# Performance work log

Measured on AMD Instinct MI355X. Metric: run time of the kernel, lower is better.

Reference implementation:

```python
import jax, jax.numpy as jnp
import numpy as np
from jax import lax

B, L, D, H = 2, 4096, 1024, 16
K = 4            # short conv kernel size
HD = D // H      # head dim = 64
EPS = 1e-5


def causal_dw_conv(x, w):
    # depthwise causal conv: x [B,L,D], w [D,K]
    xp = jnp.pad(x, ((0, 0), (K - 1, 0), (0, 0)))
    out = xp[:, 0:L, :] * w[:, 0]
    for j in range(1, K):
        out = out + xp[:, j:j + L, :] * w[:, j]
    return out


def setup_inputs() -> dict:
    key = jax.random.key(0)
    ks = jax.random.split(key, 10)
    s = 0.02
    return {
        "hidden_states": jax.random.normal(ks[0], (B, L, D), jnp.float32),
        "Wq": jax.random.normal(ks[1], (D, D), jnp.float32) * s,
        "Wk": jax.random.normal(ks[2], (D, D), jnp.float32) * s,
        "Wv": jax.random.normal(ks[3], (D, D), jnp.float32) * s,
        "Wb": jax.random.normal(ks[4], (D, H), jnp.float32) * s,
        "conv_q": jax.random.normal(ks[5], (D, K), jnp.float32) * s,
        "conv_k": jax.random.normal(ks[6], (D, K), jnp.float32) * s,
        "conv_v": jax.random.normal(ks[7], (D, K), jnp.float32) * s,
        "o_norm_w": jnp.ones((HD,), jnp.float32),
        "Wo": jax.random.normal(ks[8], (D, D), jnp.float32) * s,
    }


def reference(hidden_states, Wq, Wk, Wv, Wb, conv_q, conv_k, conv_v, o_norm_w, Wo):
    x = hidden_states
    # projections + short causal conv with SiLU (qk_activation == 'silu')
    q = jax.nn.silu(causal_dw_conv(x @ Wq, conv_q))
    k = jax.nn.silu(causal_dw_conv(x @ Wk, conv_k))
    v = jax.nn.silu(causal_dw_conv(x @ Wv, conv_v))

    # [B,L,D] -> [L,B,H,hd] for the time scan
    def to_heads(t):
        return t.reshape(B, L, H, HD).transpose(1, 0, 2, 3)

    q, k, v = to_heads(q), to_heads(k), to_heads(v)

    # l2 qk-norm
    q = q / jnp.linalg.norm(q, axis=-1, keepdims=True)
    k = k / jnp.linalg.norm(k, axis=-1, keepdims=True)

    # beta gate [L,B,H]
    beta = jax.nn.sigmoid(x @ Wb).transpose(1, 0, 2)

    def step(S, inp):
        qt, kt, vt, bt = inp  # [B,H,hd] x3, [B,H]
        v_old = jnp.einsum('bhk,bhkv->bhv', kt, S)
        delta = (vt - v_old) * bt[..., None]
        S = S + jnp.einsum('bhk,bhv->bhkv', kt, delta)
        ot = jnp.einsum('bhk,bhkv->bhv', qt, S)
        return S, ot

    S0 = jnp.zeros((B, H, HD, HD), x.dtype)
    _, o = lax.scan(step, S0, (q, k, v, beta))  # o: [L,B,H,hd]
    o = o.transpose(1, 0, 2, 3)  # [B,L,H,hd]

    # per-head RMSNorm
    rms = jax.lax.rsqrt(jnp.mean(o * o, axis=-1, keepdims=True) + EPS)
    o = o * rms * o_norm_w

    return o.reshape(B, L, D) @ Wo
```

## Files before the change

### kernel.cpp

```cpp
#include <hip/hip_runtime.h>
#include <hip/hip_bf16.h>
#include <math.h>

#define BB 2
#define LL 4096
#define DD 1024
#define HH 16
#define HDIM 64
#define CC 64
#define NC 64
#define BH 32
#define GG 8
#define GS 8

typedef __attribute__((ext_vector_type(8))) short short8;
typedef __attribute__((ext_vector_type(4))) float f32x4;
typedef unsigned short u16;

__device__ __forceinline__ u16 f2bf(float f) {
    unsigned int u = __float_as_uint(f);
    unsigned int r = (u + 0x7fffu + ((u >> 16) & 1u)) >> 16;
    return (u16)r;
}
__device__ __forceinline__ float bf2f(u16 h) {
    return __uint_as_float((unsigned)h << 16);
}
__device__ __forceinline__ void split2(float x, u16& h, u16& l) {
    h = f2bf(x);
    l = f2bf(x - bf2f(h));
}

__device__ __forceinline__ void gld_lds16(const void* g, void* l) {
    __builtin_amdgcn_global_load_lds(
        (const __attribute__((address_space(1))) void*)g,
        (__attribute__((address_space(3))) void*)l, 16, 0, 0);
}

__device__ __forceinline__ int swz(int r, int c) {
    return (r << 6) + ((((c >> 2) ^ (r >> 2)) & 15) << 2) + (c & 3);
}
__device__ __forceinline__ int swze(int r, int c) {
    return (r << 6) + (c ^ (((r ^ (r >> 3)) & 7) << 3));
}

__device__ __forceinline__ void mm64(const u16* __restrict__ Ah, const u16* __restrict__ Al,
                                     const u16* __restrict__ Bh, const u16* __restrict__ Bl,
                                     f32x4* acc, int w, int lane) {
    const int ln = lane & 15, kg = (lane >> 4) * 8;
#pragma unroll
    for (int kb = 0; kb < 2; ++kb) {
        const int k0 = kb * 32 + kg;
        short8 ah = *(const short8*)&Ah[swze(w * 16 + ln, k0)];
        short8 al = *(const short8*)&Al[swze(w * 16 + ln, k0)];
#pragma unroll
        for (int j = 0; j < 4; ++j) {
            short8 bh = *(const short8*)&Bh[swze(j * 16 + ln, k0)];
            short8 bl = *(const short8*)&Bl[swze(j * 16 + ln, k0)];
            acc[j] = __builtin_amdgcn_mfma_f32_16x16x32_bf16(ah, bh, acc[j], 0, 0, 0);
            acc[j] = __builtin_amdgcn_mfma_f32_16x16x32_bf16(ah, bl, acc[j], 0, 0, 0);
            acc[j] = __builtin_amdgcn_mfma_f32_16x16x32_bf16(al, bh, acc[j], 0, 0, 0);
        }
    }
}

__device__ __forceinline__ void g_to_ls(const float* __restrict__ G, u16* Ah, u16* Al, int tid) {
#pragma unroll
    for (int p = 0; p < 4; ++p) {
        int flat = p * 1024 + tid * 4;
        int r = flat >> 6, c = flat & 63;
        float4 v = *(const float4*)&G[flat];
        u16 h0, l0, h1, l1, h2, l2, h3, l3;
        split2(v.x, h0, l0); split2(v.y, h1, l1);
        split2(v.z, h2, l2); split2(v.w, h3, l3);
        int idx = swze(r, c);
        uint2 hv, lv;
        hv.x = (unsigned)h0 | ((unsigned)h1 << 16); hv.y = (unsigned)h2 | ((unsigned)h3 << 16);
        lv.x = (unsigned)l0 | ((unsigned)l1 << 16); lv.y = (unsigned)l2 | ((unsigned)l3 << 16);
        *(uint2*)&Ah[idx] = hv;
        *(uint2*)&Al[idx] = lv;
    }
}

__device__ __forceinline__ void frag_to_ls(const f32x4* acc, u16* Ah, u16* Al, int w, int lane) {
    const int g = lane >> 4, ln = lane & 15;
#pragma unroll
    for (int j = 0; j < 4; ++j)
#pragma unroll
        for (int r = 0; r < 4; ++r) {
            int row = w * 16 + g * 4 + r, col = j * 16 + ln;
            u16 h, l; split2(acc[j][r], h, l);
            Ah[swze(row, col)] = h;
            Al[swze(row, col)] = l;
        }
}

__device__ __forceinline__ void g_to_frag(const float* __restrict__ G, f32x4* acc, int w, int lane) {
    const int g = lane >> 4, ln = lane & 15;
#pragma unroll
    for (int j = 0; j < 4; ++j)
#pragma unroll
        for (int r = 0; r < 4; ++r)
            acc[j][r] = G[(w * 16 + g * 4 + r) * 64 + j * 16 + ln];
}
__device__ __forceinline__ void g_add_frag(const float* __restrict__ G, f32x4* acc, int w, int lane) {
    const int g = lane >> 4, ln = lane & 15;
#pragma unroll
    for (int j = 0; j < 4; ++j)
#pragma unroll
        for (int r = 0; r < 4; ++r)
            acc[j][r] += G[(w * 16 + g * 4 + r) * 64 + j * 16 + ln];
}
__device__ __forceinline__ void frag_to_g(const f32x4* acc, float* __restrict__ G, int w, int lane) {
    const int g = lane >> 4, ln = lane & 15;
#pragma unroll
    for (int j = 0; j < 4; ++j)
#pragma unroll
        for (int r = 0; r < 4; ++r)
            G[(w * 16 + g * 4 + r) * 64 + j * 16 + ln] = acc[j][r];
}

__global__ __launch_bounds__(256) void cast_bf16_k(const float* __restrict__ in,
                                                   u16* __restrict__ out) {
    int i = (blockIdx.x * 256 + threadIdx.x) * 8;
    float4 a = *(const float4*)&in[i];
    float4 b = *(const float4*)&in[i + 4];
    uint4 o;
    o.x = (unsigned)f2bf(a.x) | ((unsigned)f2bf(a.y) << 16);
    o.y = (unsigned)f2bf(a.z) | ((unsigned)f2bf(a.w) << 16);
    o.z = (unsigned)f2bf(b.x) | ((unsigned)f2bf(b.y) << 16);
    o.w = (unsigned)f2bf(b.z) | ((unsigned)f2bf(b.w) << 16);
    *(uint4*)&out[i] = o;
}

__global__ __launch_bounds__(256) void transW4_k(const float* __restrict__ W0,
                                                 const float* __restrict__ W1,
                                                 const float* __restrict__ W2,
                                                 const float* __restrict__ W3,
                                                 u16* __restrict__ WT0) {
    __shared__ float t[32][33];
    const int which = blockIdx.z;
    const float* W = (which == 0) ? W0 : (which == 1) ? W1 : (which == 2) ? W2 : W3;
    u16* WT = WT0 + (size_t)which * 1048576;
    const int bx = blockIdx.x * 32, by = blockIdx.y * 32;
#pragma unroll
    for (int p = 0; p < 4; ++p) {
        int idx = p * 256 + threadIdx.x;
        int r = idx >> 5, cc = idx & 31;
        t[r][cc] = W[(size_t)(by + r) * 1024 + bx + cc];
    }
    __syncthreads();
#pragma unroll
    for (int p = 0; p < 4; ++p) {
        int idx = p * 256 + threadIdx.x;
        int r = idx >> 5, cc = idx & 31;
        WT[(size_t)(bx + r) * 1024 + by + cc] = f2bf(t[cc][r]);
    }
}

__device__ __forceinline__ void gemm_body(const u16* A, const u16* BT,
                                          float* C, int m0, int n0) {
    __shared__ __align__(16) short As[128 * 32];
    __shared__ __align__(16) short Bs[128 * 32];
    const int tid = threadIdx.x;
    const int lane = tid & 63, w = tid >> 6;
    const int wr = w >> 1, wc = w & 1;
    const int ln15 = lane & 15, kg8 = (lane >> 4) * 8;
    f32x4 acc[4][4] = {};
    const int erow = tid >> 2;
    const int ecol = (tid & 3) * 8;
    for (int k0 = 0; k0 < 1024; k0 += 32) {
#pragma unroll
        for (int r = 0; r < 2; ++r) {
            gld_lds16(A  + (size_t)(m0 + erow + r * 64) * 1024 + k0 + ecol,
                      (short*)As + r * 2048 + tid * 8);
            gld_lds16(BT + (size_t)(n0 + erow + r * 64) * 1024 + k0 + ecol,
                      (short*)Bs + r * 2048 + tid * 8);
        }
        __syncthreads();
        short8 af[4], bf[4];
#pragma unroll
        for (int i = 0; i < 4; ++i)
            af[i] = *(const short8*)&As[(wr * 64 + i * 16 + ln15) * 32 + kg8];
#pragma unroll
        for (int j = 0; j < 4; ++j)
            bf[j] = *(const short8*)&Bs[(wc * 64 + j * 16 + ln15) * 32 + kg8];
#pragma unroll
        for (int i = 0; i < 4; ++i)
#pragma unroll
            for (int j = 0; j < 4; ++j)
                acc[i][j] = __builtin_amdgcn_mfma_f32_16x16x32_bf16(af[i], bf[j], acc[i][j], 0, 0, 0);
        __syncthreads();
    }
    const int crow0 = m0 + wr * 64 + (lane >> 4) * 4;
    const int ccol0 = n0 + wc * 64 + ln15;
#pragma unroll
    for (int i = 0; i < 4; ++i)
#pragma unroll
        for (int j = 0; j < 4; ++j)
#pragma unroll
            for (int r = 0; r < 4; ++r)
                C[(size_t)(crow0 + i * 16 + r) * 1024 + ccol0 + j * 16] = acc[i][j][r];
}

__global__ __launch_bounds__(256) void gemm_bf16(const u16* __restrict__ A,
                                                 const u16* __restrict__ BT,
                                                 float* __restrict__ C) {
    gemm_body(A, BT, C, blockIdx.y * 128, blockIdx.x * 128);
}

__global__ __launch_bounds__(256) void gemm_qkv(const u16* __restrict__ A,
                                                const u16* __restrict__ WT0,
                                                float* __restrict__ C0) {
    const int which = blockIdx.x >> 3;
    const int n0 = (blockIdx.x & 7) * 128;
    const u16* BT = WT0 + (size_t)which * 1048576;
    float* C = C0 + (size_t)which * ((size_t)BB * LL * DD);
    gemm_body(A, BT, C, blockIdx.y * 128, n0);
}

__global__ __launch_bounds__(256) void beta_k(const float* __restrict__ X,
                                              const float* __restrict__ Wb,
                                              float* __restrict__ beta) {
    int idx = blockIdx.x * 256 + threadIdx.x;
    int row = idx >> 4, h = idx & 15;
    const float* xr = X + (size_t)row * DD;
    float s = 0.f;
    for (int k4 = 0; k4 < DD; k4 += 4) {
        float4 xv = *(const float4*)&xr[k4];
        s += xv.x * Wb[(k4 + 0) * HH + h];
        s += xv.y * Wb[(k4 + 1) * HH + h];
        s += xv.z * Wb[(k4 + 2) * HH + h];
        s += xv.w * Wb[(k4 + 3) * HH + h];
    }
    float bv = 1.f / (1.f + expf(-s));
    int b = row >> 12, l = row & (LL - 1);
    beta[((size_t)b * HH + h) * LL + l] = bv;
}

__global__ __launch_bounds__(256) void conv3_k(const float* __restrict__ Xq,
                                               const float* __restrict__ Xk,
                                               const float* __restrict__ Xv,
                                               const float* __restrict__ cwq,
                                               const float* __restrict__ cwk,
                                               const float* __restrict__ cwv,
                                               float* __restrict__ oq,
                                               float* __restrict__ ok,
                                               float* __restrict__ ov) {
    const int which = blockIdx.z;
    const float* X  = (which == 0) ? Xq  : (which == 1) ? Xk  : Xv;
    const float* cw = (which == 0) ? cwq : (which == 1) ? cwk : cwv;
    float* out      = (which == 0) ? oq  : (which == 1) ? ok  : ov;
    const bool NORM = (which < 2);
    const int l0 = blockIdx.x * 16, b = blockIdx.y;
    const int tid = threadIdx.x;
    const int d0 = tid * 4;
    const float4 w0 = *(const float4*)&cw[(d0 + 0) * 4];
    const float4 w1 = *(const float4*)&cw[(d0 + 1) * 4];
    const float4 w2 = *(const float4*)&cw[(d0 + 2) * 4];
    const float4 w3 = *(const float4*)&cw[(d0 + 3) * 4];
    const float* Xb = X + (size_t)b * LL * DD;
    float4 xm3 = make_float4(0, 0, 0, 0), xm2 = xm3, xm1 = xm3;
    if (l0 > 0) {
        xm3 = *(const float4*)&Xb[(size_t)(l0 - 3) * DD + d0];
        xm2 = *(const float4*)&Xb[(size_t)(l0 - 2) * DD + d0];
        xm1 = *(const float4*)&Xb[(size_t)(l0 - 1) * DD + d0];
    }
    const int h = d0 >> 6, hd = d0 & 63;
#pragma unroll
    for (int t = 0; t < 16; ++t) {
        const int l = l0 + t;
        float4 xc = *(const float4*)&Xb[(size_t)l * DD + d0];
        float a0 = xm3.x * w0.x + xm2.x * w0.y + xm1.x * w0.z + xc.x * w0.w;
        float a1 = xm3.y * w1.x + xm2.y * w1.y + xm1.y * w1.z + xc.y * w1.w;
        float a2 = xm3.z * w2.x + xm2.z * w2.y + xm1.z * w2.z + xc.z * w2.w;
        float a3 = xm3.w * w3.x + xm2.w * w3.y + xm1.w * w3.z + xc.w * w3.w;
        a0 = a0 / (1.f + expf(-a0));
        a1 = a1 / (1.f + expf(-a1));
        a2 = a2 / (1.f + expf(-a2));
        a3 = a3 / (1.f + expf(-a3));
        if (NORM) {
            float s = a0 * a0 + a1 * a1 + a2 * a2 + a3 * a3;
            s += __shfl_xor(s, 1);
            s += __shfl_xor(s, 2);
            s += __shfl_xor(s, 4);
            s += __shfl_xor(s, 8);
            float sc = rsqrtf(s);
            a0 *= sc; a1 *= sc; a2 *= sc; a3 *= sc;
        }
        *(float4*)&out[(((size_t)b * HH + h) * LL + l) * 64 + hd] =
            make_float4(a0, a1, a2, a3);
        xm3 = xm2; xm2 = xm1; xm1 = xc;
    }
}

__global__ __launch_bounds__(256) void phaseA4(const float* __restrict__ kg,
                                               const float* __restrict__ vg,
                                               const float* __restrict__ betag,
                                               float* __restrict__ Wg,
                                               float* __restrict__ UgT,
                                               float* __restrict__ Pall,
                                               float* __restrict__ BallT) {
    __shared__ __align__(16) char pool[81920];
    u16* Kh  = (u16*)pool;
    u16* Kl  = (u16*)(pool + 8192);
    u16* KTh = (u16*)(pool + 16384);
    u16* KTl = (u16*)(pool + 24576);
    float* At = (float*)(pool + 32768);
    float* WU = (float*)(pool + 49152);
    u16* WTh = (u16*)pool;
    u16* WTl = (u16*)(pool + 8192);
    u16* UTh = (u16*)(pool + 32768);
    u16* UTl = (u16*)(pool + 40960);
    float* scr = (float*)(pool + 49152);

    const int c = blockIdx.x, bh = blockIdx.y;
    const int tid = threadIdx.x, lane = tid & 63, w = tid >> 6;
    const int g = lane >> 4, ln = lane & 15;
    const int t0 = (tid >> 4) * 4, d4 = (tid & 15) * 4;
    const size_t base = ((size_t)bh * LL + (size_t)c * 64) * 64;
    const size_t obase = ((size_t)bh * NC + c) * 4096;
    const float* bet = betag + (size_t)bh * LL + (size_t)c * 64;

    g_to_ls(&kg[base], Kh, Kl, tid);
    {
        u16 h4[4][4], l4[4][4];
#pragma unroll
        for (int i = 0; i < 4; ++i) {
            float4 v = *(const float4*)&kg[base + (size_t)(t0 + i) * 64 + d4];
            split2(v.x, h4[i][0], l4[i][0]); split2(v.y, h4[i][1], l4[i][1]);
            split2(v.z, h4[i][2], l4[i][2]); split2(v.w, h4[i][3], l4[i][3]);
        }
#pragma unroll
        for (int j = 0; j < 4; ++j) {
            uint2 hv, lv;
            hv.x = (unsigned)h4[0][j] | ((unsigned)h4[1][j] << 16);
            hv.y = (unsigned)h4[2][j] | ((unsigned)h4[3][j] << 16);
            lv.x = (unsigned)l4[0][j] | ((unsigned)l4[1][j] << 16);
            lv.y = (unsigned)l4[2][j] | ((unsigned)l4[3][j] << 16);
            *(uint2*)&KTh[swze(d4 + j, t0)] = hv;
            *(uint2*)&KTl[swze(d4 + j, t0)] = lv;
        }
    }
    __syncthreads();
    {
        f32x4 acc[4] = {};
        mm64(Kh, Kl, Kh, Kl, acc, w, lane);
#pragma unroll
        for (int r = 0; r < 4; ++r) {
            int t = w * 16 + g * 4 + r;
            float bt = bet[t];
#pragma unroll
            for (int j = 0; j < 4; ++j) {
                int s = j * 16 + ln;
                At[t * 64 + s] = (s < t) ? bt * acc[j][r] : 0.f;
            }
        }
    }
#pragma unroll
    for (int p = 0; p < 8; ++p) {
        int flat = p * 1024 + tid * 4;
        int t = flat >> 7, j = flat & 127;
        float bt = bet[t];
        float4 src;
        if (j < 64) {
            int idx = swze(t, j);
            uint2 hh = *(const uint2*)&Kh[idx];
            uint2 ll2 = *(const uint2*)&Kl[idx];
            src.x = bf2f((u16)hh.x) + bf2f((u16)ll2.x);
            src.y = bf2f((u16)(hh.x >> 16)) + bf2f((u16)(ll2.x >> 16));
            src.z = bf2f((u16)hh.y) + bf2f((u16)ll2.y);
            src.w = bf2f((u16)(hh.y >> 16)) + bf2f((u16)(ll2.y >> 16));
        } else {
            src = *(const float4*)&vg[base + (size_t)t * 64 + (j - 64)];
        }
        src.x *= bt; src.y *= bt; src.z *= bt; src.w *= bt;
        *(float4*)&WU[t * 128 + j] = src;
    }
    __syncthreads();
#pragma unroll
    for (int pb = 0; pb < 4; ++pb) {
        const int r0 = pb * 16;
        if (pb > 0) {
            const int col = tid & 127;
            const int rbase = r0 + (tid >> 7) * 8;
            float acc8[8] = {};
            for (int r = 0; r < r0; r += 4) {
                float u0 = WU[(r + 0) * 128 + col], u1 = WU[(r + 1) * 128 + col];
                float u2 = WU[(r + 2) * 128 + col], u3 = WU[(r + 3) * 128 + col];
#pragma unroll
                for (int i = 0; i < 8; ++i) {
                    float4 a4 = *(const float4*)&At[(rbase + i) * 64 + r];
                    acc8[i] += a4.x * u0 + a4.y * u1 + a4.z * u2 + a4.w * u3;
                }
            }
#pragma unroll
            for (int i = 0; i < 8; ++i) WU[(rbase + i) * 128 + col] -= acc8[i];
            __syncthreads();
        }
        if (tid < 128) {
            const int col = tid;
            float wv[16];
            wv[0] = WU[r0 * 128 + col];
#pragma unroll
            for (int t = 1; t < 16; ++t) {
                float a = WU[(r0 + t) * 128 + col];
#pragma unroll
                for (int r = 0; r < t; ++r) a -= At[(r0 + t) * 64 + r0 + r] * wv[r];
                wv[t] = a;
            }
#pragma unroll
            for (int t = 1; t < 16; ++t) WU[(r0 + t) * 128 + col] = wv[t];
        }
        __syncthreads();
    }
#pragma unroll
    for (int p = 0; p < 4; ++p) {
        int flat = p * 1024 + tid * 4;
        int t = flat >> 6, j = flat & 63;
        *(float4*)&Wg[obase + flat] = *(const float4*)&WU[t * 128 + j];
    }
    {
        u16 h4[4][4], l4[4][4];
#pragma unroll
        for (int i = 0; i < 4; ++i) {
            float4 v = *(const float4*)&WU[(t0 + i) * 128 + d4];
            split2(v.x, h4[i][0], l4[i][0]); split2(v.y, h4[i][1], l4[i][1]);
            split2(v.z, h4[i][2], l4[i][2]); split2(v.w, h4[i][3], l4[i][3]);
        }
#pragma unroll
        for (int j = 0; j < 4; ++j) {
            uint2 hv, lv;
            hv.x = (unsigned)h4[0][j] | ((unsigned)h4[1][j] << 16);
            hv.y = (unsigned)h4[2][j] | ((unsigned)h4[3][j] << 16);
            lv.x = (unsigned)l4[0][j] | ((unsigned)l4[1][j] << 16);
            lv.y = (unsigned)l4[2][j] | ((unsigned)l4[3][j] << 16);
            *(uint2*)&WTh[swze(d4 + j, t0)] = hv;
            *(uint2*)&WTl[swze(d4 + j, t0)] = lv;
        }
#pragma unroll
        for (int i = 0; i < 4; ++i) {
            float4 v = *(const float4*)&WU[(t0 + i) * 128 + 64 + d4];
            split2(v.x, h4[i][0], l4[i][0]); split2(v.y, h4[i][1], l4[i][1]);
            split2(v.z, h4[i][2], l4[i][2]); split2(v.w, h4[i][3], l4[i][3]);
        }
#pragma unroll
        for (int j = 0; j < 4; ++j) {
            uint2 hv, lv;
            hv.x = (unsigned)h4[0][j] | ((unsigned)h4[1][j] << 16);
            hv.y = (unsigned)h4[2][j] | ((unsigned)h4[3][j] << 16);
            lv.x = (unsigned)l4[0][j] | ((unsigned)l4[1][j] << 16);
            lv.y = (unsigned)l4[2][j] | ((unsigned)l4[3][j] << 16);
            *(uint2*)&UTh[swze(d4 + j, t0)] = hv;
            *(uint2*)&UTl[swze(d4 + j, t0)] = lv;
        }
    }
    __syncthreads();
#pragma unroll
    for (int p = 0; p < 4; ++p) {
        int flat = p * 1024 + tid * 4;
        int n = flat >> 6, tt = flat & 63;
        int idx = swze(n, tt);
        uint2 hh = *(const uint2*)&UTh[idx];
        uint2 ll2 = *(const uint2*)&UTl[idx];
        float4 o;
        o.x = bf2f((u16)hh.x) + bf2f((u16)ll2.x);
        o.y = bf2f((u16)(hh.x >> 16)) + bf2f((u16)(ll2.x >> 16));
        o.z = bf2f((u16)hh.y) + bf2f((u16)ll2.y);
        o.w = bf2f((u16)(hh.y >> 16)) + bf2f((u16)(ll2.y >> 16));
        *(float4*)&UgT[obase + flat] = o;
    }
    f32x4 aP[4] = {}, aB[4] = {};
    mm64(KTh, KTl, WTh, WTl, aP, w, lane);
    mm64(KTh, KTl, UTh, UTl, aB, w, lane);
#pragma unroll
    for (int j = 0; j < 4; ++j)
#pragma unroll
        for (int r = 0; r < 4; ++r) {
            int row = w * 16 + g * 4 + r, col = j * 16 + ln;
            float pv = ((row == col) ? 1.f : 0.f) - aP[j][r];
            Pall[obase + (size_t)row * 64 + col] = pv;
            scr[swz(row, col)] = aB[j][r];
        }
    __syncthreads();
#pragma unroll
    for (int p = 0; p < 4; ++p) {
        int flat = p * 1024 + tid * 4;
        int n = flat >> 6, dd = flat & 63;
        float4 o;
        o.x = scr[swz(dd + 0, n)];
        o.y = scr[swz(dd + 1, n)];
        o.z = scr[swz(dd + 2, n)];
        o.w = scr[swz(dd + 3, n)];
        *(float4*)&BallT[obase + flat] = o;
    }
}

__global__ __launch_bounds__(256) void compose3(const float* __restrict__ Pall,
                                                const float* __restrict__ BallT,
                                                float* __restrict__ Pg,
                                                float* __restrict__ BgT) {
    __shared__ __align__(16) char pool[81920];
    u16* Ph = (u16*)pool;
    u16* Pl = (u16*)(pool + 8192);
    u16* Bh = (u16*)(pool + 16384);
    u16* Bl = (u16*)(pool + 24576);
    u16* nh = (u16*)(pool + 32768);
    u16* nl = (u16*)(pool + 40960);
    float* scr = (float*)(pool + 49152);
    const int g = blockIdx.x, bh = blockIdx.y;
    const int tid = threadIdx.x, lane = tid & 63, w = tid >> 6;
    const int gi = lane >> 4, ln = lane & 15;
    const size_t base0 = ((size_t)bh * NC + (size_t)g * GS) * 4096;
    f32x4 mP[4], mB[4];
#pragma unroll
    for (int p = 0; p < 4; ++p) {
        int flat = p * 1024 + tid * 4;
        int r = flat >> 6, c4 = flat & 63;
        *(float4*)&scr[swz(r, c4)] = *(const float4*)&Pall[base0 + flat];
    }
    g_to_frag(BallT + base0, mB, w, lane);
    __syncthreads();
#pragma unroll
    for (int j = 0; j < 4; ++j)
#pragma unroll
        for (int r = 0; r < 4; ++r) {
            int row = w * 16 + gi * 4 + r, col = j * 16 + ln;
            mP[j][r] = scr[swz(col, row)];
        }
    for (int s = 1; s < GS; ++s) {
        __syncthreads();
        frag_to_ls(mP, Ph, Pl, w, lane);
        frag_to_ls(mB, Bh, Bl, w, lane);
        g_to_ls(&Pall[base0 + (size_t)s * 4096], nh, nl, tid);
        __syncthreads();
        f32x4 aP[4] = {}, aB[4] = {};
        mm64(Ph, Pl, nh, nl, aP, w, lane);
        mm64(Bh, Bl, nh, nl, aB, w, lane);
        g_add_frag(&BallT[base0 + (size_t)s * 4096], aB, w, lane);
#pragma unroll
        for (int j = 0; j < 4; ++j) { mP[j] = aP[j]; mB[j] = aB[j]; }
    }
    const size_t gbase = ((size_t)bh * GG + g) * 4096;
    frag_to_g(mB, BgT + gbase, w, lane);
    __syncthreads();
#pragma unroll
    for (int j = 0; j < 4; ++j)
#pragma unroll
        for (int r = 0; r < 4; ++r) {
            int row = w * 16 + gi * 4 + r, col = j * 16 + ln;
            scr[swz(row, col)] = mP[j][r];
        }
    __syncthreads();
#pragma unroll
    for (int p = 0; p < 4; ++p) {
        int flat = p * 1024 + tid * 4;
        int a = flat >> 6, b0 = flat & 63;
        float4 o;
        o.x = scr[swz(b0 + 0, a)];
        o.y = scr[swz(b0 + 1, a)];
        o.z = scr[swz(b0 + 2, a)];
        o.w = scr[swz(b0 + 3, a)];
        *(float4*)&Pg[gbase + flat] = o;
    }
}

__global__ __launch_bounds__(256) void scanG3(const float* __restrict__ Pg,
                                              const float* __restrict__ BgT,
                                              float* __restrict__ SallT) {
    __shared__ __align__(16) char pool[32768];
    u16* Sh = (u16*)pool;
    u16* Sl = (u16*)(pool + 8192);
    u16* nh = (u16*)(pool + 16384);
    u16* nl = (u16*)(pool + 24576);
    const int bh = blockIdx.x;
    const int tid = threadIdx.x, lane = tid & 63, w = tid >> 6;
    f32x4 mS[4] = {};
    for (int g = 0; g < GG; ++g) {
        const size_t sbase = ((size_t)bh * NC + (size_t)g * GS) * 4096;
        frag_to_g(mS, SallT + sbase, w, lane);
        if (g == GG - 1) break;
        __syncthreads();
        frag_to_ls(mS, Sh, Sl, w, lane);
        g_to_ls(&Pg[((size_t)bh * GG + g) * 4096], nh, nl, tid);
        __syncthreads();
        f32x4 a[4] = {};
        mm64(Sh, Sl, nh, nl, a, w, lane);
        g_add_frag(&BgT[((size_t)bh * GG + g) * 4096], a, w, lane);
#pragma unroll
        for (int j = 0; j < 4; ++j) mS[j] = a[j];
    }
}

__global__ __launch_bounds__(256) void rollout3(const float* __restrict__ Pall,
                                                const float* __restrict__ BallT,
                                                float* __restrict__ SallT) {
    __shared__ __align__(16) char pool[32768];
    u16* Sh = (u16*)pool;
    u16* Sl = (u16*)(pool + 8192);
    u16* nh = (u16*)(pool + 16384);
    u16* nl = (u16*)(pool + 24576);
    const int g = blockIdx.x, bh = blockIdx.y;
    const int tid = threadIdx.x, lane = tid & 63, w = tid >> 6;
    const size_t base0 = ((size_t)bh * NC + (size_t)g * GS) * 4096;
    f32x4 mS[4];
    g_to_frag(SallT + base0, mS, w, lane);
    for (int j = 1; j < GS; ++j) {
        __syncthreads();
        frag_to_ls(mS, Sh, Sl, w, lane);
        g_to_ls(&Pall[base0 + (size_t)(j - 1) * 4096], nh, nl, tid);
        __syncthreads();
        f32x4 a[4] = {};
        mm64(Sh, Sl, nh, nl, a, w, lane);
        g_add_frag(&BallT[base0 + (size_t)(j - 1) * 4096], a, w, lane);
#pragma unroll
        for (int jj = 0; jj < 4; ++jj) mS[jj] = a[jj];
        frag_to_g(mS, SallT + base0 + (size_t)j * 4096, w, lane);
    }
}

__global__ __launch_bounds__(256) void phaseO3(const float* __restrict__ Wg,
                                               const float* __restrict__ UgT,
                                               const float* __restrict__ qg,
                                               const float* __restrict__ kg,
                                               const float* __restrict__ SallT,
                                               const float* __restrict__ nw,
                                               u16* __restrict__ ob) {
    __shared__ __align__(16) char pool[65536];
    u16* Qh = (u16*)pool;
    u16* Ql = (u16*)(pool + 8192);
    u16* Kh = (u16*)(pool + 16384);
    u16* Kl = (u16*)(pool + 24576);
    u16* Wh = (u16*)(pool + 32768);
    u16* Wl = (u16*)(pool + 40960);
    u16* Sh = (u16*)(pool + 49152);
    u16* Sl = (u16*)(pool + 57344);
    u16* Dh = Kh; u16* Dl = Kl;
    u16* Mh = Wh; u16* Ml = Wl;
    const int c = blockIdx.x, bh = blockIdx.y;
    const int b = bh >> 4, h = bh & 15;
    const int tid = threadIdx.x, lane = tid & 63, w = tid >> 6;
    const int gi = lane >> 4, ln = lane & 15;
    const size_t tbase = ((size_t)bh * NC + c) * 4096;
    const size_t qkbase = ((size_t)bh * LL + (size_t)c * 64) * 64;
    g_to_ls(&qg[qkbase], Qh, Ql, tid);
    g_to_ls(&kg[qkbase], Kh, Kl, tid);
    g_to_ls(&Wg[tbase], Wh, Wl, tid);
    g_to_ls(&SallT[tbase], Sh, Sl, tid);
    __syncthreads();
    f32x4 aM[4] = {}, aD[4] = {};
    mm64(Qh, Ql, Kh, Kl, aM, w, lane);
    mm64(Sh, Sl, Wh, Wl, aD, w, lane);
    __syncthreads();
#pragma unroll
    for (int j = 0; j < 4; ++j)
#pragma unroll
        for (int r = 0; r < 4; ++r) {
            int row = w * 16 + gi * 4 + r, col = j * 16 + ln;
            float mv = (col <= row) ? aM[j][r] : 0.f;
            u16 mh_, ml_; split2(mv, mh_, ml_);
            Mh[swze(row, col)] = mh_;
            Ml[swze(row, col)] = ml_;
            float dv = UgT[tbase + (size_t)row * 64 + col] - aD[j][r];
            u16 dh_, dl_; split2(dv, dh_, dl_);
            Dh[swze(row, col)] = dh_;
            Dl[swze(row, col)] = dl_;
        }
    __syncthreads();
    f32x4 aO[4] = {};
    mm64(Qh, Ql, Sh, Sl, aO, w, lane);
    mm64(Mh, Ml, Dh, Dl, aO, w, lane);
    float nwv[4];
#pragma unroll
    for (int j = 0; j < 4; ++j) nwv[j] = nw[j * 16 + ln];
#pragma unroll
    for (int r = 0; r < 4; ++r) {
        float ss = 0.f;
#pragma unroll
        for (int j = 0; j < 4; ++j) ss += aO[j][r] * aO[j][r];
        ss += __shfl_xor(ss, 1);
        ss += __shfl_xor(ss, 2);
        ss += __shfl_xor(ss, 4);
        ss += __shfl_xor(ss, 8);
        float rms = rsqrtf(ss * (1.f / 64.f) + 1e-5f);
        int row = w * 16 + gi * 4 + r;
        size_t orow = ((size_t)b * LL + (size_t)c * 64 + row) * DD + (size_t)h * 64;
#pragma unroll
        for (int j = 0; j < 4; ++j)
            ob[orow + j * 16 + ln] = f2bf(aO[j][r] * rms * nwv[j]);
    }
}

extern "C" void kernel_launch(void* const* d_in, const int* in_sizes, int n_in,
                              void* d_out, int out_size, void* d_ws, size_t ws_size,
                              hipStream_t stream) {
    const float* x  = (const float*)d_in[0];
    const float* Wq = (const float*)d_in[1];
    const float* Wk = (const float*)d_in[2];
    const float* Wv = (const float*)d_in[3];
    const float* Wb = (const float*)d_in[4];
    const float* cq = (const float*)d_in[5];
    const float* ck = (const float*)d_in[6];
    const float* cv = (const float*)d_in[7];
    const float* nw = (const float*)d_in[8];
    const float* Wo = (const float*)d_in[9];
    float* out = (float*)d_out;
    float* ws = (float*)d_ws;

    const size_t SZ = (size_t)BB * LL * DD;
    float* xq   = ws;
    float* xk   = ws + SZ;
    float* xv   = ws + 2 * SZ;
    float* q    = ws + 3 * SZ;
    float* k    = ws + 4 * SZ;
    float* v    = ws + 5 * SZ;
    float* beta = ws + 6 * SZ;
    u16* wqT = (u16*)(beta + (size_t)BH * LL);
    float* SallT = (float*)wqT + 2097152;
    float* PgB  = SallT + SZ;
    float* BgT  = PgB + 1048576;

    u16* xb = (u16*)q;
    u16* ob = (u16*)v;
    u16* woT = wqT + (size_t)3 * 1048576;
    float* Wg = xq;
    float* UgT = xk;
    float* Pall = xv;
    float* BallT = out;

    dim3 blk(256);

    cast_bf16_k<<<dim3(4096), blk, 0, stream>>>(x, xb);
    transW4_k<<<dim3(32, 32, 4), blk, 0, stream>>>(Wq, Wk, Wv, Wo, wqT);
    gemm_qkv<<<dim3(24, 64), blk, 0, stream>>>(xb, wqT, xq);
    beta_k<<<dim3(512), blk, 0, stream>>>(x, Wb, beta);
    conv3_k<<<dim3(LL / 16, BB, 3), blk, 0, stream>>>(xq, xk, xv, cq, ck, cv, q, k, v);
    phaseA4<<<dim3(NC, BH), blk, 0, stream>>>(k, v, beta, Wg, UgT, Pall, BallT);
    compose3<<<dim3(GG, BH), blk, 0, stream>>>(Pall, BallT, PgB, BgT);
    scanG3<<<dim3(BH), blk, 0, stream>>>(PgB, BgT, SallT);
    rollout3<<<dim3(GG, BH), blk, 0, stream>>>(Pall, BallT, SallT);
    phaseO3<<<dim3(NC, BH), blk, 0, stream>>>(Wg, UgT, q, k, SallT, nw, ob);
    gemm_bf16<<<dim3(8, 64), blk, 0, stream>>>(ob, woT, out);
}
```

Measured before the change: 387.0 us.

## Store q/k intermediates in bf16 and drop split-precision MFMA terms for them

The QKV GEMM now writes the q and k projections as bf16, the conv kernel reads bf16 and writes normalized q/k as bf16, and the chunk kernels load them directly without hi/lo splitting. Products involving only q/k use a single bf16 MFMA instead of three, and mixed products use two. This cuts memory traffic, LDS footprint and MFMA count in conv, phaseA and phaseO. The GEMM LDS tiles also gain an XOR swizzle to reduce bank conflicts. The cost is lower precision in q/k, which risks accuracy drift through the recurrent delta-rule state.

Result: faster. 363.1 us (-6.2%).

```diff
diff --git a/kernel.cpp b/kernel.cpp
--- a/kernel.cpp
+++ b/kernel.cpp
@@ -29,6 +29,11 @@
     h = f2bf(x);
     l = f2bf(x - bf2f(h));
 }
+__device__ __forceinline__ float4 ld_bf4(const u16* p) {
+    uint2 v = *(const uint2*)p;
+    return make_float4(bf2f((u16)v.x), bf2f((u16)(v.x >> 16)),
+                       bf2f((u16)v.y), bf2f((u16)(v.y >> 16)));
+}
 
 __device__ __forceinline__ void gld_lds16(const void* g, void* l) {
     __builtin_amdgcn_global_load_lds(
@@ -59,6 +64,38 @@
             acc[j] = __builtin_amdgcn_mfma_f32_16x16x32_bf16(ah, bh, acc[j], 0, 0, 0);
             acc[j] = __builtin_amdgcn_mfma_f32_16x16x32_bf16(ah, bl, acc[j], 0, 0, 0);
             acc[j] = __builtin_amdgcn_mfma_f32_16x16x32_bf16(al, bh, acc[j], 0, 0, 0);
+        }
+    }
+}
+__device__ __forceinline__ void mm64_bb(const u16* __restrict__ Ah,
+                                        const u16* __restrict__ Bh,
+                                        f32x4* acc, int w, int lane) {
+    const int ln = lane & 15, kg = (lane >> 4) * 8;
+#pragma unroll
+    for (int kb = 0; kb < 2; ++kb) {
+        const int k0 = kb * 32 + kg;
+        short8 ah = *(const short8*)&Ah[swze(w * 16 + ln, k0)];
+#pragma unroll
+        for (int j = 0; j < 4; ++j) {
+            short8 bh = *(const short8*)&Bh[swze(j * 16 + ln, k0)];
+            acc[j] = __builtin_amdgcn_mfma_f32_16x16x32_bf16(ah, bh, acc[j], 0, 0, 0);
+        }
+    }
+}
+__device__ __forceinline__ void mm64_ab(const u16* __restrict__ Ah,
+                                        const u16* __restrict__ Bh, const u16* __restrict__ Bl,
+                                        f32x4* acc, int w, int lane) {
+    const int ln = lane & 15, kg = (lane >> 4) * 8;
+#pragma unroll
+    for (int kb = 0; kb < 2; ++kb) {
+        const int k0 = kb * 32 + kg;
+        short8 ah = *(const short8*)&Ah[swze(w * 16 + ln, k0)];
+#pragma unroll
+        for (int j = 0; j < 4; ++j) {
+            short8 bh = *(const short8*)&Bh[swze(j * 16 + ln, k0)];
+            short8 bl = *(const short8*)&Bl[swze(j * 16 + ln, k0)];
+            acc[j] = __builtin_amdgcn_mfma_f32_16x16x32_bf16(ah, bh, acc[j], 0, 0, 0);
+            acc[j] = __builtin_amdgcn_mfma_f32_16x16x32_bf16(ah, bl, acc[j], 0, 0, 0);
         }
     }
 }
@@ -80,6 +117,14 @@
         *(uint2*)&Al[idx] = lv;
     }
 }
+__device__ __forceinline__ void g_to_ls_b(const u16* __restrict__ G16, u16* Ah, int tid) {
+#pragma unroll
+    for (int p = 0; p < 2; ++p) {
+        int flat = p * 2048 + tid * 8;
+        int r = flat >> 6, c = flat & 63;
+        *(short8*)&Ah[swze(r, c)] = *(const short8*)&G16[flat];
+    }
+}
 
 __device__ __forceinline__ void frag_to_ls(const f32x4* acc, u16* Ah, u16* Al, int w, int lane) {
     const int g = lane >> 4, ln = lane & 15;
@@ -157,17 +202,17 @@
     }
 }
 
-__device__ __forceinline__ void gemm_body(const u16* A, const u16* BT,
-                                          float* C, int m0, int n0) {
+__device__ __forceinline__ void gemm_core(const u16* A, const u16* BT,
+                                          int m0, int n0, f32x4 acc[4][4]) {
     __shared__ __align__(16) short As[128 * 32];
     __shared__ __align__(16) short Bs[128 * 32];
     const int tid = threadIdx.x;
     const int lane = tid & 63, w = tid >> 6;
     const int wr = w >> 1, wc = w & 1;
-    const int ln15 = lane & 15, kg8 = (lane >> 4) * 8;
-    f32x4 acc[4][4] = {};
+    const int ln15 = lane & 15;
     const int erow = tid >> 2;
-    const int ecol = (tid & 3) * 8;
+    const int ecol = (((tid & 3) ^ ((erow >> 1) & 3)) << 3);
+    const int kch = lane >> 4;
     for (int k0 = 0; k0 < 1024; k0 += 32) {
 #pragma unroll
         for (int r = 0; r < 2; ++r) {
@@ -179,11 +224,15 @@
         __syncthreads();
         short8 af[4], bf[4];
 #pragma unroll
-        for (int i = 0; i < 4; ++i)
-            af[i] = *(const short8*)&As[(wr * 64 + i * 16 + ln15) * 32 + kg8];
-#pragma unroll
-        for (int j = 0; j < 4; ++j)
-            bf[j] = *(const short8*)&Bs[(wc * 64 + j * 16 + ln15) * 32 + kg8];
+        for (int i = 0; i < 4; ++i) {
+            int row = wr * 64 + i * 16 + ln15;
+            af[i] = *(const short8*)&As[row * 32 + ((kch ^ ((row >> 1) & 3)) << 3)];
+        }
+#pragma unroll
+        for (int j = 0; j < 4; ++j) {
+            int row = wc * 64 + j * 16 + ln15;
+            bf[j] = *(const short8*)&Bs[row * 32 + ((kch ^ ((row >> 1) & 3)) << 3)];
+        }
 #pragma unroll
         for (int i = 0; i < 4; ++i)
 #pragma unroll
@@ -191,31 +240,58 @@
                 acc[i][j] = __builtin_amdgcn_mfma_f32_16x16x32_bf16(af[i], bf[j], acc[i][j], 0, 0, 0);
         __syncthreads();
     }
-    const int crow0 = m0 + wr * 64 + (lane >> 4) * 4;
-    const int ccol0 = n0 + wc * 64 + ln15;
-#pragma unroll
-    for (int i = 0; i < 4; ++i)
-#pragma unroll
-        for (int j = 0; j < 4; ++j)
-#pragma unroll
-            for (int r = 0; r < 4; ++r)
-                C[(size_t)(crow0 + i * 16 + r) * 1024 + ccol0 + j * 16] = acc[i][j][r];
 }
 
 __global__ __launch_bounds__(256) void gemm_bf16(const u16* __restrict__ A,
                                                  const u16* __restrict__ BT,
                                                  float* __restrict__ C) {
-    gemm_body(A, BT, C, blockIdx.y * 128, blockIdx.x * 128);
+    const int m0 = blockIdx.y * 128, n0 = blockIdx.x * 128;
+    f32x4 acc[4][4] = {};
+    gemm_core(A, BT, m0, n0, acc);
+    const int lane = threadIdx.x & 63, w = threadIdx.x >> 6;
+    const int crow0 = m0 + (w >> 1) * 64 + (lane >> 4) * 4;
+    const int ccol0 = n0 + (w & 1) * 64 + (lane & 15);
+#pragma unroll
+    for (int i = 0; i < 4; ++i)
+#pragma unroll
+        for (int j = 0; j < 4; ++j)
+#pragma unroll
+            for (int r = 0; r < 4; ++r)
+                C[(size_t)(crow0 + i * 16 + r) * 1024 + ccol0 + j * 16] = acc[i][j][r];
 }
 
 __global__ __launch_bounds__(256) void gemm_qkv(const u16* __restrict__ A,
                                                 const u16* __restrict__ WT0,
-                                                float* __restrict__ C0) {
+                                                u16* __restrict__ xq16,
+                                                u16* __restrict__ xk16,
+                                                float* __restrict__ xv) {
     const int which = blockIdx.x >> 3;
     const int n0 = (blockIdx.x & 7) * 128;
+    const int m0 = blockIdx.y * 128;
     const u16* BT = WT0 + (size_t)which * 1048576;
-    float* C = C0 + (size_t)which * ((size_t)BB * LL * DD);
-    gemm_body(A, BT, C, blockIdx.y * 128, n0);
+    f32x4 acc[4][4] = {};
+    gemm_core(A, BT, m0, n0, acc);
+    const int lane = threadIdx.x & 63, w = threadIdx.x >> 6;
+    const int crow0 = m0 + (w >> 1) * 64 + (lane >> 4) * 4;
+    const int ccol0 = n0 + (w & 1) * 64 + (lane & 15);
+    if (which == 2) {
+#pragma unroll
+        for (int i = 0; i < 4; ++i)
+#pragma unroll
+            for (int j = 0; j < 4; ++j)
+#pragma unroll
+                for (int r = 0; r < 4; ++r)
+                    xv[(size_t)(crow0 + i * 16 + r) * 1024 + ccol0 + j * 16] = acc[i][j][r];
+    } else {
+        u16* C16 = (which == 0) ? xq16 : xk16;
+#pragma unroll
+        for (int i = 0; i < 4; ++i)
+#pragma unroll
+            for (int j = 0; j < 4; ++j)
+#pragma unroll
+                for (int r = 0; r < 4; ++r)
+                    C16[(size_t)(crow0 + i * 16 + r) * 1024 + ccol0 + j * 16] = f2bf(acc[i][j][r]);
+    }
 }
 
 __global__ __launch_bounds__(256) void beta_k(const float* __restrict__ X,
@@ -237,20 +313,17 @@
     beta[((size_t)b * HH + h) * LL + l] = bv;
 }
 
-__global__ __launch_bounds__(256) void conv3_k(const float* __restrict__ Xq,
-                                               const float* __restrict__ Xk,
-                                               const float* __restrict__ Xv,
+__global__ __launch_bounds__(256) void conv3_k(const u16* __restrict__ xq16,
+                                               const u16* __restrict__ xk16,
+                                               const float* __restrict__ xv,
                                                const float* __restrict__ cwq,
                                                const float* __restrict__ cwk,
                                                const float* __restrict__ cwv,
-                                               float* __restrict__ oq,
-                                               float* __restrict__ ok,
-                                               float* __restrict__ ov) {
+                                               u16* __restrict__ q16,
+                                               u16* __restrict__ k16,
+                                               float* __restrict__ vout) {
     const int which = blockIdx.z;
-    const float* X  = (which == 0) ? Xq  : (which == 1) ? Xk  : Xv;
     const float* cw = (which == 0) ? cwq : (which == 1) ? cwk : cwv;
-    float* out      = (which == 0) ? oq  : (which == 1) ? ok  : ov;
-    const bool NORM = (which < 2);
     const int l0 = blockIdx.x * 16, b = blockIdx.y;
     const int tid = threadIdx.x;
     const int d0 = tid * 4;
@@ -258,27 +331,28 @@
     const float4 w1 = *(const float4*)&cw[(d0 + 1) * 4];
     const float4 w2 = *(const float4*)&cw[(d0 + 2) * 4];
     const float4 w3 = *(const float4*)&cw[(d0 + 3) * 4];
-    const float* Xb = X + (size_t)b * LL * DD;
-    float4 xm3 = make_float4(0, 0, 0, 0), xm2 = xm3, xm1 = xm3;
-    if (l0 > 0) {
-        xm3 = *(const float4*)&Xb[(size_t)(l0 - 3) * DD + d0];
-        xm2 = *(const float4*)&Xb[(size_t)(l0 - 2) * DD + d0];
-        xm1 = *(const float4*)&Xb[(size_t)(l0 - 1) * DD + d0];
-    }
     const int h = d0 >> 6, hd = d0 & 63;
-#pragma unroll
-    for (int t = 0; t < 16; ++t) {
-        const int l = l0 + t;
-        float4 xc = *(const float4*)&Xb[(size_t)l * DD + d0];
-        float a0 = xm3.x * w0.x + xm2.x * w0.y + xm1.x * w0.z + xc.x * w0.w;
-        float a1 = xm3.y * w1.x + xm2.y * w1.y + xm1.y * w1.z + xc.y * w1.w;
-        float a2 = xm3.z * w2.x + xm2.z * w2.y + xm1.z * w2.z + xc.z * w2.w;
-        float a3 = xm3.w * w3.x + xm2.w * w3.y + xm1.w * w3.z + xc.w * w3.w;
-        a0 = a0 / (1.f + expf(-a0));
-        a1 = a1 / (1.f + expf(-a1));
-        a2 = a2 / (1.f + expf(-a2));
-        a3 = a3 / (1.f + expf(-a3));
-        if (NORM) {
+    if (which < 2) {
+        const u16* Xb = ((which == 0) ? xq16 : xk16) + (size_t)b * LL * DD;
+        u16* O16 = (which == 0) ? q16 : k16;
+        float4 xm3 = make_float4(0, 0, 0, 0), xm2 = xm3, xm1 = xm3;
+        if (l0 > 0) {
+            xm3 = ld_bf4(&Xb[(size_t)(l0 - 3) * DD + d0]);
+            xm2 = ld_bf4(&Xb[(size_t)(l0 - 2) * DD + d0]);
+            xm1 = ld_bf4(&Xb[(size_t)(l0 - 1) * DD + d0]);
+        }
+#pragma unroll
+        for (int t = 0; t < 16; ++t) {
+            const int l = l0 + t;
+            float4 xc = ld_bf4(&Xb[(size_t)l * DD + d0]);
+            float a0 = xm3.x * w0.x + xm2.x * w0.y + xm1.x * w0.z + xc.x * w0.w;
+            float a1 = xm3.y * w1.x + xm2.y * w1.y + xm1.y * w1.z + xc.y * w1.w;
+            float a2 = xm3.z * w2.x + xm2.z * w2.y + xm1.z * w2.z + xc.z * w2.w;
+            float a3 = xm3.w * w3.x + xm2.w * w3.y + xm1.w * w3.z + xc.w * w3.w;
+            a0 = a0 / (1.f + expf(-a0));
+            a1 = a1 / (1.f + expf(-a1));
+            a2 = a2 / (1.f + expf(-a2));
+            a3 = a3 / (1.f + expf(-a3));
             float s = a0 * a0 + a1 * a1 + a2 * a2 + a3 * a3;
             s += __shfl_xor(s, 1);
             s += __shfl_xor(s, 2);
@@ -286,32 +360,56 @@
             s += __shfl_xor(s, 8);
             float sc = rsqrtf(s);
             a0 *= sc; a1 *= sc; a2 *= sc; a3 *= sc;
-        }
-        *(float4*)&out[(((size_t)b * HH + h) * LL + l) * 64 + hd] =
-            make_float4(a0, a1, a2, a3);
-        xm3 = xm2; xm2 = xm1; xm1 = xc;
-    }
-}
-
-__global__ __launch_bounds__(256) void phaseA4(const float* __restrict__ kg,
+            uint2 o;
+            o.x = (unsigned)f2bf(a0) | ((unsigned)f2bf(a1) << 16);
+            o.y = (unsigned)f2bf(a2) | ((unsigned)f2bf(a3) << 16);
+            *(uint2*)&O16[(((size_t)b * HH + h) * LL + l) * 64 + hd] = o;
+            xm3 = xm2; xm2 = xm1; xm1 = xc;
+        }
+    } else {
+        const float* Xb = xv + (size_t)b * LL * DD;
+        float4 xm3 = make_float4(0, 0, 0, 0), xm2 = xm3, xm1 = xm3;
+        if (l0 > 0) {
+            xm3 = *(const float4*)&Xb[(size_t)(l0 - 3) * DD + d0];
+            xm2 = *(const float4*)&Xb[(size_t)(l0 - 2) * DD + d0];
+            xm1 = *(const float4*)&Xb[(size_t)(l0 - 1) * DD + d0];
+        }
+#pragma unroll
+        for (int t = 0; t < 16; ++t) {
+            const int l = l0 + t;
+            float4 xc = *(const float4*)&Xb[(size_t)l * DD + d0];
+            float a0 = xm3.x * w0.x + xm2.x * w0.y + xm1.x * w0.z + xc.x * w0.w;
+            float a1 = xm3.y * w1.x + xm2.y * w1.y + xm1.y * w1.z + xc.y * w1.w;
+            float a2 = xm3.z * w2.x + xm2.z * w2.y + xm1.z * w2.z + xc.z * w2.w;
+            float a3 = xm3.w * w3.x + xm2.w * w3.y + xm1.w * w3.z + xc.w * w3.w;
+            a0 = a0 / (1.f + expf(-a0));
+            a1 = a1 / (1.f + expf(-a1));
+            a2 = a2 / (1.f + expf(-a2));
+            a3 = a3 / (1.f + expf(-a3));
+            *(float4*)&vout[(((size_t)b * HH + h) * LL + l) * 64 + hd] =
+                make_float4(a0, a1, a2, a3);
+            xm3 = xm2; xm2 = xm1; xm1 = xc;
+        }
+    }
+}
+
+__global__ __launch_bounds__(256) void phaseA5(const u16* __restrict__ kg16,
                                                const float* __restrict__ vg,
                                                const float* __restrict__ betag,
                                                float* __restrict__ Wg,
                                                float* __restrict__ UgT,
                                                float* __restrict__ Pall,
                                                float* __restrict__ BallT) {
-    __shared__ __align__(16) char pool[81920];
-    u16* Kh  = (u16*)pool;
-    u16* Kl  = (u16*)(pool + 8192);
-    u16* KTh = (u16*)(pool + 16384);
-    u16* KTl = (u16*)(pool + 24576);
-    float* At = (float*)(pool + 32768);
-    float* WU = (float*)(pool + 49152);
-    u16* WTh = (u16*)pool;
-    u16* WTl = (u16*)(pool + 8192);
-    u16* UTh = (u16*)(pool + 32768);
-    u16* UTl = (u16*)(pool + 40960);
-    float* scr = (float*)(pool + 49152);
+    __shared__ __align__(16) char pool[73728];
+    u16* Kh   = (u16*)pool;
+    u16* KTh  = (u16*)(pool + 8192);
+    float* At = (float*)(pool + 16384);
+    float* WU = (float*)(pool + 32768);
+    u16* WTh  = (u16*)pool;
+    u16* WTl  = (u16*)(pool + 16384);
+    u16* UTh  = (u16*)(pool + 24576);
+    u16* UTl  = (u16*)(pool + 65536);
+    float* scr = (float*)(pool + 32768);
 
     const int c = blockIdx.x, bh = blockIdx.y;
     const int tid = threadIdx.x, lane = tid & 63, w = tid >> 6;
@@ -321,30 +419,27 @@
     const size_t obase = ((size_t)bh * NC + c) * 4096;
     const float* bet = betag + (size_t)bh * LL + (size_t)c * 64;
 
-    g_to_ls(&kg[base], Kh, Kl, tid);
+    g_to_ls_b(kg16 + base, Kh, tid);
     {
-        u16 h4[4][4], l4[4][4];
+        u16 kv[4][4];
 #pragma unroll
         for (int i = 0; i < 4; ++i) {
-            float4 v = *(const float4*)&kg[base + (size_t)(t0 + i) * 64 + d4];
-            split2(v.x, h4[i][0], l4[i][0]); split2(v.y, h4[i][1], l4[i][1]);
-            split2(v.z, h4[i][2], l4[i][2]); split2(v.w, h4[i][3], l4[i][3]);
+            uint2 v = *(const uint2*)&kg16[base + (size_t)(t0 + i) * 64 + d4];
+            kv[i][0] = (u16)v.x; kv[i][1] = (u16)(v.x >> 16);
+            kv[i][2] = (u16)v.y; kv[i][3] = (u16)(v.y >> 16);
         }
 #pragma unroll
         for (int j = 0; j < 4; ++j) {
-            uint2 hv, lv;
-            hv.x = (unsigned)h4[0][j] | ((unsigned)h4[1][j] << 16);
-            hv.y = (unsigned)h4[2][j] | ((unsigned)h4[3][j] << 16);
-            lv.x = (unsigned)l4[0][j] | ((unsigned)l4[1][j] << 16);
-            lv.y = (unsigned)l4[2][j] | ((unsigned)l4[3][j] << 16);
+            uint2 hv;
+            hv.x = (unsigned)kv[0][j] | ((unsigned)kv[1][j] << 16);
+            hv.y = (unsigned)kv[2][j] | ((unsigned)kv[3][j] << 16);
             *(uint2*)&KTh[swze(d4 + j, t0)] = hv;
-            *(uint2*)&KTl[swze(d4 + j, t0)] = lv;
         }
     }
     __syncthreads();
     {
         f32x4 acc[4] = {};
-        mm64(Kh, Kl, Kh, Kl, acc, w, lane);
+        mm64_bb(Kh, Kh, acc, w, lane);
 #pragma unroll
         for (int r = 0; r < 4; ++r) {
             int t = w * 16 + g * 4 + r;
@@ -362,17 +457,8 @@
         int t = flat >> 7, j = flat & 127;
         float bt = bet[t];
         float4 src;
-        if (j < 64) {
-            int idx = swze(t, j);
-            uint2 hh = *(const uint2*)&Kh[idx];
-            uint2 ll2 = *(const uint2*)&Kl[idx];
-            src.x = bf2f((u16)hh.x) + bf2f((u16)ll2.x);
-            src.y = bf2f((u16)(hh.x >> 16)) + bf2f((u16)(ll2.x >> 16));
-            src.z = bf2f((u16)hh.y) + bf2f((u16)ll2.y);
-            src.w = bf2f((u16)(hh.y >> 16)) + bf2f((u16)(ll2.y >> 16));
-        } else {
-            src = *(const float4*)&vg[base + (size_t)t * 64 + (j - 64)];
-        }
+        if (j < 64) src = ld_bf4(&Kh[swze(t, j)]);
+        else        src = *(const float4*)&vg[base + (size_t)t * 64 + (j - 64)];
         src.x *= bt; src.y *= bt; src.z *= bt; src.w *= bt;
         *(float4*)&WU[t * 128 + j] = src;
     }
@@ -470,8 +556,8 @@
         *(float4*)&UgT[obase + flat] = o;
     }
     f32x4 aP[4] = {}, aB[4] = {};
-    mm64(KTh, KTl, WTh, WTl, aP, w, lane);
-    mm64(KTh, KTl, UTh, UTl, aB, w, lane);
+    mm64_ab(KTh, WTh, WTl, aP, w, lane);
+    mm64_ab(KTh, UTh, UTl, aB, w, lane);
 #pragma unroll
     for (int j = 0; j < 4; ++j)
 #pragma unroll
@@ -618,23 +704,22 @@
     }
 }
 
-__global__ __launch_bounds__(256) void phaseO3(const float* __restrict__ Wg,
+__global__ __launch_bounds__(256) void phaseO4(const float* __restrict__ Wg,
                                                const float* __restrict__ UgT,
-                                               const float* __restrict__ qg,
-                                               const float* __restrict__ kg,
+                                               const u16* __restrict__ qg16,
+                                               const u16* __restrict__ kg16,
                                                const float* __restrict__ SallT,
                                                const float* __restrict__ nw,
                                                u16* __restrict__ ob) {
-    __shared__ __align__(16) char pool[65536];
+    __shared__ __align__(16) char pool[57344];
     u16* Qh = (u16*)pool;
-    u16* Ql = (u16*)(pool + 8192);
-    u16* Kh = (u16*)(pool + 16384);
-    u16* Kl = (u16*)(pool + 24576);
-    u16* Wh = (u16*)(pool + 32768);
-    u16* Wl = (u16*)(pool + 40960);
-    u16* Sh = (u16*)(pool + 49152);
-    u16* Sl = (u16*)(pool + 57344);
-    u16* Dh = Kh; u16* Dl = Kl;
+    u16* Kh = (u16*)(pool + 8192);
+    u16* Wh = (u16*)(pool + 16384);
+    u16* Wl = (u16*)(pool + 24576);
+    u16* Sh = (u16*)(pool + 32768);
+    u16* Sl = (u16*)(pool + 40960);
+    u16* Dl = (u16*)(pool + 49152);
+    u16* Dh = Kh;
     u16* Mh = Wh; u16* Ml = Wl;
     const int c = blockIdx.x, bh = blockIdx.y;
     const int b = bh >> 4, h = bh & 15;
@@ -642,13 +727,13 @@
     const int gi = lane >> 4, ln = lane & 15;
     const size_t tbase = ((size_t)bh * NC + c) * 4096;
     const size_t qkbase = ((size_t)bh * LL + (size_t)c * 64) * 64;
-    g_to_ls(&qg[qkbase], Qh, Ql, tid);
-    g_to_ls(&kg[qkbase], Kh, Kl, tid);
+    g_to_ls_b(qg16 + qkbase, Qh, tid);
+    g_to_ls_b(kg16 + qkbase, Kh, tid);
     g_to_ls(&Wg[tbase], Wh, Wl, tid);
     g_to_ls(&SallT[tbase], Sh, Sl, tid);
     __syncthreads();
     f32x4 aM[4] = {}, aD[4] = {};
-    mm64(Qh, Ql, Kh, Kl, aM, w, lane);
+    mm64_bb(Qh, Kh, aM, w, lane);
     mm64(Sh, Sl, Wh, Wl, aD, w, lane);
     __syncthreads();
 #pragma unroll
@@ -667,7 +752,7 @@
         }
     __syncthreads();
     f32x4 aO[4] = {};
-    mm64(Qh, Ql, Sh, Sl, aO, w, lane);
+    mm64_ab(Qh, Sh, Sl, aO, w, lane);
     mm64(Mh, Ml, Dh, Dl, aO, w, lane);
     float nwv[4];
 #pragma unroll
@@ -707,37 +792,37 @@
     float* ws = (float*)d_ws;
 
     const size_t SZ = (size_t)BB * LL * DD;
-    float* xq   = ws;
-    float* xk   = ws + SZ;
-    float* xv   = ws + 2 * SZ;
-    float* q    = ws + 3 * SZ;
-    float* k    = ws + 4 * SZ;
-    float* v    = ws + 5 * SZ;
-    float* beta = ws + 6 * SZ;
-    u16* wqT = (u16*)(beta + (size_t)BH * LL);
-    float* SallT = (float*)wqT + 2097152;
-    float* PgB  = SallT + SZ;
-    float* BgT  = PgB + 1048576;
-
-    u16* xb = (u16*)q;
-    u16* ob = (u16*)v;
-    u16* woT = wqT + (size_t)3 * 1048576;
-    float* Wg = xq;
-    float* UgT = xk;
-    float* Pall = xv;
+    float* xv    = ws;
+    float* v     = ws + SZ;
+    float* Wg    = ws + 2 * SZ;
+    float* UgT   = ws + 3 * SZ;
+    float* SallT = ws + 4 * SZ;
+    u16* xb   = (u16*)(ws + 5 * SZ);
+    u16* q16  = xb;
+    u16* xq16 = (u16*)(ws + 5 * SZ) + SZ;
+    u16* xk16 = (u16*)(ws + 5 * SZ) + 2 * SZ;
+    u16* k16  = (u16*)(ws + 5 * SZ) + 3 * SZ;
+    float* beta = ws + 7 * SZ;
+    u16* wqT  = (u16*)(beta + (size_t)BH * LL);
+    float* PgB = (float*)(wqT + (size_t)4 * 1048576);
+    float* BgT = PgB + 1048576;
+
+    float* Pall  = xv;
     float* BallT = out;
+    u16* ob   = (u16*)v;
+    u16* woT  = wqT + (size_t)3 * 1048576;
 
     dim3 blk(256);
 
     cast_bf16_k<<<dim3(4096), blk, 0, stream>>>(x, xb);
     transW4_k<<<dim3(32, 32, 4), blk, 0, stream>>>(Wq, Wk, Wv, Wo, wqT);
-    gemm_qkv<<<dim3(24, 64), blk, 0, stream>>>(xb, wqT, xq);
+    gemm_qkv<<<dim3(24, 64), blk, 0, stream>>>(xb, wqT, xq16, xk16, xv);
     beta_k<<<dim3(512), blk, 0, stream>>>(x, Wb, beta);
-    conv3_k<<<dim3(LL / 16, BB, 3), blk, 0, stream>>>(xq, xk, xv, cq, ck, cv, q, k, v);
-    phaseA4<<<dim3(NC, BH), blk, 0, stream>>>(k, v, beta, Wg, UgT, Pall, BallT);
+    conv3_k<<<dim3(LL / 16, BB, 3), blk, 0, stream>>>(xq16, xk16, xv, cq, ck, cv, q16, k16, v);
+    phaseA5<<<dim3(NC, BH), blk, 0, stream>>>(k16, v, beta, Wg, UgT, Pall, BallT);
     compose3<<<dim3(GG, BH), blk, 0, stream>>>(Pall, BallT, PgB, BgT);
     scanG3<<<dim3(BH), blk, 0, stream>>>(PgB, BgT, SallT);
     rollout3<<<dim3(GG, BH), blk, 0, stream>>>(Pall, BallT, SallT);
-    phaseO3<<<dim3(NC, BH), blk, 0, stream>>>(Wg, UgT, q, k, SallT, nw, ob);
+    phaseO4<<<dim3(NC, BH), blk, 0, stream>>>(Wg, UgT, q16, k16, SallT, nw, ob);
     gemm_bf16<<<dim3(8, 64), blk, 0, stream>>>(ob, woT, out);
 }
```
